# Kernel optimization log

Measured on AMD Instinct MI355X. Metric: run time of the kernel, lower is better.

The kernel has to match this reference:

```python
import jax, jax.numpy as jnp
import numpy as np

D_MODEL = 1024
N_HEADS = 16
HEAD_DIM = 64
INNER = N_HEADS * HEAD_DIM
D_FF = 4096


def ln_novar(x, w, b):
    # mean-only 'layernorm' (no variance division), per original LayerNormNoVar
    u = jnp.mean(x, axis=-1, keepdims=True)
    return w * (x - u) + b


def setup_inputs() -> dict:
    key = jax.random.key(0)
    ks = jax.random.split(key, 12)
    s = lambda k, shape, scale: jax.random.normal(k, shape, dtype=jnp.float32) * scale
    inp = {
        "src": s(ks[0], (4, 2048, D_MODEL), 1.0),
        "pre_norm_w": jnp.ones((D_MODEL,), jnp.float32),
        "pre_norm_b": jnp.zeros((D_MODEL,), jnp.float32),
        "wq": s(ks[1], (D_MODEL, INNER), 0.02),
        "wk": s(ks[2], (D_MODEL, INNER), 0.02),
        "wv": s(ks[3], (D_MODEL, INNER), 0.02),
        "w_proj": s(ks[4], (INNER, D_MODEL), 0.02),
        "b_proj": jnp.zeros((D_MODEL,), jnp.float32),
        "norm1_w": jnp.ones((D_MODEL,), jnp.float32),
        "norm1_b": jnp.zeros((D_MODEL,), jnp.float32),
        "w1": s(ks[5], (D_MODEL, D_FF), 0.02),
        "b1": jnp.zeros((D_FF,), jnp.float32),
        "w2": s(ks[6], (D_FF, D_MODEL), 0.02),
        "b2": jnp.zeros((D_MODEL,), jnp.float32),
    }
    return inp


def reference(src, pre_norm_w, pre_norm_b, wq, wk, wv, w_proj, b_proj,
              norm1_w, norm1_b, w1, b1, w2, b2):
    B, N, _ = src.shape
    scale = HEAD_DIM ** -0.5
    x = ln_novar(src, pre_norm_w, pre_norm_b)
    q = (x @ wq).reshape(B, N, N_HEADS, HEAD_DIM)
    k = (x @ wk).reshape(B, N, N_HEADS, HEAD_DIM)
    v = (x @ wv).reshape(B, N, N_HEADS, HEAD_DIM)
    attn = jnp.einsum('bqhd,bkhd->bhqk', q, k) * scale
    attn = jax.nn.softmax(attn, axis=-1)
    o = jnp.einsum('bhqk,bkhd->bqhd', attn, v).reshape(B, N, INNER)
    o = o @ w_proj + b_proj
    src = src + o
    src = ln_novar(src, norm1_w, norm1_b)
    ff = jax.nn.relu(src @ w1 + b1) @ w2 + b2
    return src + ff
```

## Files before the change

kernel.cpp:

```cpp
#include <hip/hip_runtime.h>
#include <hip/hip_bf16.h>
#include <stdint.h>

typedef __hip_bfloat16 bf16;
typedef float f32x4 __attribute__((ext_vector_type(4)));
typedef float f32x16 __attribute__((ext_vector_type(16)));
typedef short v8s __attribute__((ext_vector_type(8)));
typedef __bf16 v8bf __attribute__((ext_vector_type(8)));
typedef unsigned int v4u __attribute__((ext_vector_type(4)));
typedef unsigned int u32;

static constexpr int MROWS = 8192;
static constexpr int DM    = 1024;
static constexpr int DFF   = 4096;
static constexpr int SEQ   = 2048;

__device__ __forceinline__ f32x4 mfma16(v8s a, v8s b, f32x4 c) {
  return __builtin_amdgcn_mfma_f32_16x16x32_bf16(
      __builtin_bit_cast(v8bf, a), __builtin_bit_cast(v8bf, b), c, 0, 0, 0);
}
__device__ __forceinline__ f32x16 mfma32(v8s a, v8s b, f32x16 c) {
  return __builtin_amdgcn_mfma_f32_32x32x16_bf16(
      __builtin_bit_cast(v8bf, a), __builtin_bit_cast(v8bf, b), c, 0, 0, 0);
}

__device__ __forceinline__ void gload_lds16(const void* g, void* l) {
  __builtin_amdgcn_global_load_lds(
      (const __attribute__((address_space(1))) void*)g,
      (__attribute__((address_space(3))) void*)l, 16, 0, 0);
}

__device__ __forceinline__ u32 cvtpk_bf16(float a, float b) {
  u32 r;
  asm("v_cvt_pk_bf16_f32 %0, %1, %2" : "=v"(r) : "v"(a), "v"(b));
  return r;
}
__device__ __forceinline__ void pl32swap(u32& x, u32& y) {
  asm volatile("v_permlane32_swap_b32 %0, %1" : "+v"(x), "+v"(y));
}
__device__ __forceinline__ float fast_exp2(float x) {
  float r;
  asm("v_exp_f32 %0, %1" : "=v"(r) : "v"(x));
  return r;
}

__global__ __launch_bounds__(256) void transpose_cast(
    const float* __restrict__ W, bf16* __restrict__ WT, int K, int N) {
  __shared__ float tile[32][33];
  const int c0 = blockIdx.x * 32;
  const int r0 = blockIdx.y * 32;
  const int tx = threadIdx.x & 31, ty = threadIdx.x >> 5;
  #pragma unroll
  for (int i = 0; i < 32; i += 8)
    tile[ty + i][tx] = W[(size_t)(r0 + ty + i) * N + c0 + tx];
  __syncthreads();
  #pragma unroll
  for (int i = 0; i < 32; i += 8)
    WT[(size_t)(c0 + ty + i) * K + r0 + tx] = __float2bfloat16(tile[tx][ty + i]);
}

__global__ __launch_bounds__(256) void ln_novar_kernel(
    const float* __restrict__ x, const float* __restrict__ w,
    const float* __restrict__ b, bf16* __restrict__ ob, float* __restrict__ of) {
  const int row = blockIdx.x;
  const int t = threadIdx.x;
  const float4 v = ((const float4*)(x + (size_t)row * DM))[t];
  float s = v.x + v.y + v.z + v.w;
  #pragma unroll
  for (int off = 32; off > 0; off >>= 1) s += __shfl_down(s, off, 64);
  __shared__ float wsum[4];
  if ((t & 63) == 0) wsum[t >> 6] = s;
  __syncthreads();
  const float u = (wsum[0] + wsum[1] + wsum[2] + wsum[3]) * (1.0f / DM);
  const float4 wv = ((const float4*)w)[t];
  const float4 bv = ((const float4*)b)[t];
  const float o0 = wv.x * (v.x - u) + bv.x;
  const float o1 = wv.y * (v.y - u) + bv.y;
  const float o2 = wv.z * (v.z - u) + bv.z;
  const float o3 = wv.w * (v.w - u) + bv.w;
  bf16* op = ob + (size_t)row * DM + t * 4;
  op[0] = __float2bfloat16(o0); op[1] = __float2bfloat16(o1);
  op[2] = __float2bfloat16(o2); op[3] = __float2bfloat16(o3);
  if (of) {
    float4 o4; o4.x = o0; o4.y = o1; o4.z = o2; o4.w = o3;
    ((float4*)(of + (size_t)row * DM))[t] = o4;
  }
}

#define BM 128
#define BN 128
#define BK 64
template <int EPI>
__global__ __launch_bounds__(256) void gemm_bt(
    const bf16* __restrict__ A, const bf16* __restrict__ BT,
    bf16* __restrict__ Cb, float* __restrict__ Cf,
    const float* __restrict__ bias, const float* __restrict__ res,
    int M, int Nn, int K) {
  __shared__ __align__(16) bf16 As[BM * BK];
  __shared__ __align__(16) bf16 Bs[BN * BK];

  const int tid = threadIdx.x;
  const int lane = tid & 63;
  const int wave = tid >> 6;
  const int wr = wave >> 1, wc = wave & 1;
  const int tM = blockIdx.y * BM, tN = blockIdx.x * BN;

  f32x4 acc[4][4] = {};

  const int nk = K / BK;
  for (int kt = 0; kt < nk; ++kt) {
    if (kt) __syncthreads();
    const int k0 = kt * BK;
    #pragma unroll
    for (int c = 0; c < 4; ++c) {
      const int slot = tid + c * 256;
      const int row = slot >> 3, s = slot & 7;
      const int kk = ((s ^ (row & 7)) << 3);
      gload_lds16(A + (size_t)(tM + row) * K + k0 + kk, (void*)(As + slot * 8));
      gload_lds16(BT + (size_t)(tN + row) * K + k0 + kk, (void*)(Bs + slot * 8));
    }
    __syncthreads();
    #pragma unroll
    for (int kk = 0; kk < 2; ++kk) {
      const int kslot = kk * 4 + (lane >> 4);
      v8s af[4], bfr[4];
      #pragma unroll
      for (int m = 0; m < 4; ++m) {
        const int row = wr * 64 + m * 16 + (lane & 15);
        af[m] = *(const v8s*)(As + (row * 8 + (kslot ^ (row & 7))) * 8);
      }
      #pragma unroll
      for (int n = 0; n < 4; ++n) {
        const int row = wc * 64 + n * 16 + (lane & 15);
        bfr[n] = *(const v8s*)(Bs + (row * 8 + (kslot ^ (row & 7))) * 8);
      }
      #pragma unroll
      for (int m = 0; m < 4; ++m)
        #pragma unroll
        for (int n = 0; n < 4; ++n)
          acc[m][n] = mfma16(af[m], bfr[n], acc[m][n]);
    }
  }

  #pragma unroll
  for (int m = 0; m < 4; ++m) {
    #pragma unroll
    for (int n = 0; n < 4; ++n) {
      const int row0 = tM + wr * 64 + m * 16 + ((lane >> 4) << 2);
      const int col = tN + wc * 64 + n * 16 + (lane & 15);
      #pragma unroll
      for (int r = 0; r < 4; ++r) {
        const size_t idx = (size_t)(row0 + r) * Nn + col;
        float v = acc[m][n][r];
        if (EPI == 0) {
          Cb[idx] = __float2bfloat16(v);
        } else if (EPI == 1) {
          v += bias[col];
          v = fmaxf(v, 0.0f);
          Cb[idx] = __float2bfloat16(v);
        } else {
          v += bias[col] + res[idx];
          Cf[idx] = v;
        }
      }
    }
  }
}

__global__ __launch_bounds__(256) void repack_kv(
    const bf16* __restrict__ qkv, bf16* __restrict__ krep,
    bf16* __restrict__ vrep) {
  const int bhkt = blockIdx.x;
  const int bh = bhkt >> 5, kt = bhkt & 31;
  const int b = bh >> 4, h = bh & 15;
  const size_t obase = (size_t)bhkt * 4096;
  #pragma unroll
  for (int it = 0; it < 16; ++it) {
    const int o = it * 256 + threadIdx.x;
    const int ch = o >> 9, rowi = (o >> 3) & 63, e = o & 7;
    krep[obase + o] =
        qkv[(size_t)(b * SEQ + kt * 64 + rowi) * 3072 + 1024 + h * 64 + ch * 8 + e];
    vrep[obase + o] =
        qkv[(size_t)(b * SEQ + kt * 64 + ch * 8 + e) * 3072 + 2048 + h * 64 + rowi];
  }
}

#define PPV(i) ((i) < 16 ? s0[(i) & 15] : s1[(i) & 15])
__global__ __launch_bounds__(256, 4) void attn_kernel(
    const bf16* __restrict__ qkv, const bf16* __restrict__ krep,
    const bf16* __restrict__ vrep, bf16* __restrict__ ob) {
  const int qt = blockIdx.x & 15;
  const int bh = blockIdx.x >> 4;
  const int b = bh >> 4, h = bh & 15;
  const int tid = threadIdx.x;
  const int lane = tid & 63, wave = tid >> 6;
  const int c = lane & 31, hi = lane >> 5;
  const float CEXP = 0.180336880111120426f;

  __shared__ __align__(16) bf16 Ks[2][4096];
  __shared__ __align__(16) bf16 Vs[2][4096];

  const int qrow = qt * 128 + wave * 32 + c;
  const bf16* qp = qkv + (size_t)(b * SEQ + qrow) * 3072 + h * 64;
  v8s qf[4];
  #pragma unroll
  for (int ks = 0; ks < 4; ++ks)
    qf[ks] = *(const v8s*)(qp + ks * 16 + hi * 8);

  f32x16 o0 = {}, o1 = {};
  float mrow = -1e30f, lrow = 0.0f;

  const size_t tilebase = (size_t)(bh * 32) * 4096;
  #pragma unroll
  for (int j = 0; j < 2; ++j) {
    gload_lds16(krep + tilebase + (tid + j * 256) * 8, &Ks[0][(tid + j * 256) * 8]);
    gload_lds16(vrep + tilebase + (tid + j * 256) * 8, &Vs[0][(tid + j * 256) * 8]);
  }
  asm volatile("s_waitcnt vmcnt(0)" ::: "memory");
  __builtin_amdgcn_s_barrier();
  asm volatile("" ::: "memory");

  for (int kt = 0; kt < 32; ++kt) {
    const int cur = kt & 1;
    if (kt < 31) {
      const size_t nb = tilebase + (size_t)(kt + 1) * 4096;
      #pragma unroll
      for (int j = 0; j < 2; ++j) {
        gload_lds16(krep + nb + (tid + j * 256) * 8, &Ks[cur ^ 1][(tid + j * 256) * 8]);
        gload_lds16(vrep + nb + (tid + j * 256) * 8, &Vs[cur ^ 1][(tid + j * 256) * 8]);
      }
    }
    const bf16* KB = Ks[cur];
    const bf16* VB = Vs[cur];

    f32x16 s0 = {}, s1 = {};
    __builtin_amdgcn_s_setprio(1);
    #pragma unroll
    for (int ks = 0; ks < 4; ++ks) {
      const int ch = (2 * ks + hi) * 512;
      v8s a0 = *(const v8s*)(KB + ch + c * 8);
      v8s a1 = *(const v8s*)(KB + ch + (c + 32) * 8);
      s0 = mfma32(a0, qf[ks], s0);
      s1 = mfma32(a1, qf[ks], s1);
    }
    __builtin_amdgcn_s_setprio(0);

    float mA = -1e30f, mB = -1e30f;
    #pragma unroll
    for (int i = 0; i < 16; i += 2) {
      mA = fmaxf(fmaxf(s0[i], s0[i + 1]), mA);
      mB = fmaxf(fmaxf(s1[i], s1[i + 1]), mB);
    }
    float tmax = fmaxf(mA, mB);
    tmax = fmaxf(tmax, __shfl_xor(tmax, 32, 64));
    if (__any(tmax - mrow > 64.0f)) {
      const float mnew = fmaxf(mrow, tmax);
      const float ef = fast_exp2((mrow - mnew) * CEXP);
      mrow = mnew;
      lrow *= ef;
      #pragma unroll
      for (int r = 0; r < 16; ++r) {
        const float efq = __shfl(ef, (r & 3) + 8 * (r >> 2) + 4 * hi, 64);
        o0[r] *= efq;
        o1[r] *= efq;
      }
    }
    const float nmc = -mrow * CEXP;
    float rs0 = 0.0f, rs1 = 0.0f;
    #pragma unroll
    for (int i = 0; i < 16; ++i) {
      s0[i] = fast_exp2(fmaf(s0[i], CEXP, nmc));
      s1[i] = fast_exp2(fmaf(s1[i], CEXP, nmc));
      rs0 += s0[i];
      rs1 += s1[i];
    }
    float rs = rs0 + rs1;
    rs += __shfl_xor(rs, 32, 64);
    lrow += rs;

    v8s pa[4];
    #pragma unroll
    for (int ks = 0; ks < 4; ++ks) {
      u32 x  = cvtpk_bf16(PPV(8 * ks + 0), PPV(8 * ks + 1));
      u32 y  = cvtpk_bf16(PPV(8 * ks + 4), PPV(8 * ks + 5));
      u32 x2 = cvtpk_bf16(PPV(8 * ks + 2), PPV(8 * ks + 3));
      u32 y2 = cvtpk_bf16(PPV(8 * ks + 6), PPV(8 * ks + 7));
      pl32swap(x, y);
      pl32swap(x2, y2);
      v4u w; w.x = x; w.y = x2; w.z = y; w.w = y2;
      pa[ks] = __builtin_bit_cast(v8s, w);
    }

    __builtin_amdgcn_s_setprio(1);
    #pragma unroll
    for (int ks = 0; ks < 4; ++ks) {
      const int ch = (2 * ks + hi) * 512;
      v8s b0 = *(const v8s*)(VB + ch + c * 8);
      v8s b1 = *(const v8s*)(VB + ch + (c + 32) * 8);
      o0 = mfma32(pa[ks], b0, o0);
      o1 = mfma32(pa[ks], b1, o1);
    }
    __builtin_amdgcn_s_setprio(0);

    asm volatile("s_waitcnt vmcnt(0)" ::: "memory");
    __builtin_amdgcn_s_barrier();
    asm volatile("" ::: "memory");
  }

  const float rl = 1.0f / lrow;
  const size_t orow0 = (size_t)(b * SEQ + qt * 128 + wave * 32);
  #pragma unroll
  for (int r = 0; r < 16; ++r) {
    const int q = (r & 3) + 8 * (r >> 2) + 4 * hi;
    const float rq = __shfl(rl, q, 64);
    bf16* op = ob + (orow0 + q) * DM + h * 64;
    op[c] = __float2bfloat16(o0[r] * rq);
    op[32 + c] = __float2bfloat16(o1[r] * rq);
  }
}

extern "C" void kernel_launch(void* const* d_in, const int* in_sizes, int n_in,
                              void* d_out, int out_size, void* d_ws,
                              size_t ws_size, hipStream_t stream) {
  const float* src   = (const float*)d_in[0];
  const float* pnw   = (const float*)d_in[1];
  const float* pnb   = (const float*)d_in[2];
  const float* wq    = (const float*)d_in[3];
  const float* wk    = (const float*)d_in[4];
  const float* wv    = (const float*)d_in[5];
  const float* wproj = (const float*)d_in[6];
  const float* bproj = (const float*)d_in[7];
  const float* n1w   = (const float*)d_in[8];
  const float* n1b   = (const float*)d_in[9];
  const float* w1    = (const float*)d_in[10];
  const float* b1    = (const float*)d_in[11];
  const float* w2    = (const float*)d_in[12];
  const float* b2    = (const float*)d_in[13];
  float* out = (float*)d_out;

  char* ws = (char*)d_ws;
  size_t off = 0;
  bf16* WTqkv = (bf16*)(ws + off); off += (size_t)3072 * 1024 * 2;
  bf16* WTprj = (bf16*)(ws + off); off += (size_t)1024 * 1024 * 2;
  bf16* WT1   = (bf16*)(ws + off); off += (size_t)4096 * 1024 * 2;
  bf16* WT2   = (bf16*)(ws + off); off += (size_t)1024 * 4096 * 2;
  bf16* xb    = (bf16*)(ws + off); off += (size_t)MROWS * DM * 2;
  bf16* qkvb  = (bf16*)(ws + off); off += (size_t)MROWS * 3072 * 2;
  bf16* obuf  = (bf16*)(ws + off); off += (size_t)MROWS * DM * 2;
  float* yf   = (float*)(ws + off); off += (size_t)MROWS * DM * 4;
  bf16* h1    = (bf16*)(ws + off); off += (size_t)MROWS * DFF * 2;
  bf16* krep = h1;
  bf16* vrep = h1 + (size_t)64 * SEQ * 64;

  const dim3 blk(256);

  transpose_cast<<<dim3(32, 32), blk, 0, stream>>>(wq, WTqkv, 1024, 1024);
  transpose_cast<<<dim3(32, 32), blk, 0, stream>>>(wk, WTqkv + 1024 * 1024, 1024, 1024);
  transpose_cast<<<dim3(32, 32), blk, 0, stream>>>(wv, WTqkv + 2048 * 1024, 1024, 1024);
  transpose_cast<<<dim3(32, 32), blk, 0, stream>>>(wproj, WTprj, 1024, 1024);
  transpose_cast<<<dim3(128, 32), blk, 0, stream>>>(w1, WT1, 1024, 4096);
  transpose_cast<<<dim3(32, 128), blk, 0, stream>>>(w2, WT2, 4096, 1024);

  ln_novar_kernel<<<MROWS, blk, 0, stream>>>(src, pnw, pnb, xb, nullptr);

  gemm_bt<0><<<dim3(3072 / BN, MROWS / BM), blk, 0, stream>>>(
      xb, WTqkv, qkvb, nullptr, nullptr, nullptr, MROWS, 3072, 1024);

  repack_kv<<<dim3(64 * 32), blk, 0, stream>>>(qkvb, krep, vrep);

  attn_kernel<<<dim3(16 * 64), dim3(256), 0, stream>>>(qkvb, krep, vrep, obuf);

  gemm_bt<2><<<dim3(1024 / BN, MROWS / BM), blk, 0, stream>>>(
      obuf, WTprj, nullptr, yf, bproj, src, MROWS, 1024, 1024);

  ln_novar_kernel<<<MROWS, blk, 0, stream>>>(yf, n1w, n1b, xb, out);

  gemm_bt<1><<<dim3(4096 / BN, MROWS / BM), blk, 0, stream>>>(
      xb, WT1, h1, nullptr, b1, nullptr, MROWS, 4096, 1024);

  gemm_bt<2><<<dim3(1024 / BN, MROWS / BM), blk, 0, stream>>>(
      h1, WT2, nullptr, out, b2, out, MROWS, 1024, 4096);
}
```

Before: 461.7 us.

## Double-buffer GEMM LDS tiles and remap blocks for XCD/L2 locality

The GEMM kernel now keeps two LDS buffers. It issues the global-to-LDS loads for the next K tile before computing on the current one, so memory latency overlaps with MFMA work and one barrier per iteration is removed. The grid becomes 1D, and block IDs are remapped in two steps: first across the 8 XCDs, then grouped 4 M-tiles per column group, so neighbouring blocks share A/B tiles in cache. The cost is double the LDS per block (64KB), which may lower occupancy.

```diff
diff --git a/kernel.cpp b/kernel.cpp
--- a/kernel.cpp
+++ b/kernel.cpp
@@ -96,30 +96,48 @@
     bf16* __restrict__ Cb, float* __restrict__ Cf,
     const float* __restrict__ bias, const float* __restrict__ res,
     int M, int Nn, int K) {
-  __shared__ __align__(16) bf16 As[BM * BK];
-  __shared__ __align__(16) bf16 Bs[BN * BK];
+  __shared__ __align__(16) bf16 As[2][BM * BK];
+  __shared__ __align__(16) bf16 Bs[2][BN * BK];
 
   const int tid = threadIdx.x;
   const int lane = tid & 63;
   const int wave = tid >> 6;
   const int wr = wave >> 1, wc = wave & 1;
-  const int tM = blockIdx.y * BM, tN = blockIdx.x * BN;
+
+  const int nwg = gridDim.x;
+  const int nbx = Nn / BN;
+  int bid = (blockIdx.x & 7) * (nwg >> 3) + (blockIdx.x >> 3);
+  const int GM = 4;
+  const int grp = bid / (GM * nbx);
+  const int rem = bid - grp * (GM * nbx);
+  const int by = grp * GM + (rem & (GM - 1));
+  const int bx = rem >> 2;
+  const int tM = by * BM, tN = bx * BN;
 
   f32x4 acc[4][4] = {};
-
   const int nk = K / BK;
-  for (int kt = 0; kt < nk; ++kt) {
-    if (kt) __syncthreads();
+
+  auto STAGE = [&](int buf, int kt) {
     const int k0 = kt * BK;
     #pragma unroll
     for (int c = 0; c < 4; ++c) {
       const int slot = tid + c * 256;
       const int row = slot >> 3, s = slot & 7;
       const int kk = ((s ^ (row & 7)) << 3);
-      gload_lds16(A + (size_t)(tM + row) * K + k0 + kk, (void*)(As + slot * 8));
-      gload_lds16(BT + (size_t)(tN + row) * K + k0 + kk, (void*)(Bs + slot * 8));
-    }
-    __syncthreads();
+      gload_lds16(A + (size_t)(tM + row) * K + k0 + kk, (void*)(&As[buf][0] + slot * 8));
+      gload_lds16(BT + (size_t)(tN + row) * K + k0 + kk, (void*)(&Bs[buf][0] + slot * 8));
+    }
+  };
+
+  STAGE(0, 0);
+  asm volatile("s_waitcnt vmcnt(0)" ::: "memory");
+  __builtin_amdgcn_s_barrier();
+  asm volatile("" ::: "memory");
+
+  for (int kt = 0; kt < nk; ++kt) {
+    const int cur = kt & 1;
+    if (kt + 1 < nk) STAGE(cur ^ 1, kt + 1);
+
     #pragma unroll
     for (int kk = 0; kk < 2; ++kk) {
       const int kslot = kk * 4 + (lane >> 4);
@@ -127,12 +145,12 @@
       #pragma unroll
       for (int m = 0; m < 4; ++m) {
         const int row = wr * 64 + m * 16 + (lane & 15);
-        af[m] = *(const v8s*)(As + (row * 8 + (kslot ^ (row & 7))) * 8);
+        af[m] = *(const v8s*)(&As[cur][0] + (row * 8 + (kslot ^ (row & 7))) * 8);
       }
       #pragma unroll
       for (int n = 0; n < 4; ++n) {
         const int row = wc * 64 + n * 16 + (lane & 15);
-        bfr[n] = *(const v8s*)(Bs + (row * 8 + (kslot ^ (row & 7))) * 8);
+        bfr[n] = *(const v8s*)(&Bs[cur][0] + (row * 8 + (kslot ^ (row & 7))) * 8);
       }
       #pragma unroll
       for (int m = 0; m < 4; ++m)
@@ -140,6 +158,10 @@
         for (int n = 0; n < 4; ++n)
           acc[m][n] = mfma16(af[m], bfr[n], acc[m][n]);
     }
+
+    asm volatile("s_waitcnt vmcnt(0)" ::: "memory");
+    __builtin_amdgcn_s_barrier();
+    asm volatile("" ::: "memory");
   }
 
   #pragma unroll
@@ -363,21 +385,21 @@
 
   ln_novar_kernel<<<MROWS, blk, 0, stream>>>(src, pnw, pnb, xb, nullptr);
 
-  gemm_bt<0><<<dim3(3072 / BN, MROWS / BM), blk, 0, stream>>>(
+  gemm_bt<0><<<dim3((3072 / BN) * (MROWS / BM)), blk, 0, stream>>>(
       xb, WTqkv, qkvb, nullptr, nullptr, nullptr, MROWS, 3072, 1024);
 
   repack_kv<<<dim3(64 * 32), blk, 0, stream>>>(qkvb, krep, vrep);
 
   attn_kernel<<<dim3(16 * 64), dim3(256), 0, stream>>>(qkvb, krep, vrep, obuf);
 
-  gemm_bt<2><<<dim3(1024 / BN, MROWS / BM), blk, 0, stream>>>(
+  gemm_bt<2><<<dim3((1024 / BN) * (MROWS / BM)), blk, 0, stream>>>(
       obuf, WTprj, nullptr, yf, bproj, src, MROWS, 1024, 1024);
 
   ln_novar_kernel<<<MROWS, blk, 0, stream>>>(yf, n1w, n1b, xb, out);
 
-  gemm_bt<1><<<dim3(4096 / BN, MROWS / BM), blk, 0, stream>>>(
+  gemm_bt<1><<<dim3((4096 / BN) * (MROWS / BM)), blk, 0, stream>>>(
       xb, WT1, h1, nullptr, b1, nullptr, MROWS, 4096, 1024);
 
-  gemm_bt<2><<<dim3(1024 / BN, MROWS / BM), blk, 0, stream>>>(
+  gemm_bt<2><<<dim3((1024 / BN) * (MROWS / BM)), blk, 0, stream>>>(
       h1, WT2, nullptr, out, b2, out, MROWS, 1024, 4096);
 }
```

New measurement: 426.5 us. 7.6% less time.
